# Optimization experiments

Measured on AMD Instinct MI355X. Metric: run time of the kernel, lower is better.

## Reference

```python
import jax, jax.numpy as jnp
import numpy as np
from math import sqrt

N = 50000      # n_nodes
M = 800000     # n_edges (avg degree 16)
D = 256        # d_Embedding
H = 8          # heads
DK = 32        # per-head key/query dim
DV = 32        # per-head value dim


def setup_inputs() -> dict:
    key = jax.random.key(0)
    ks = jax.random.split(key, 10)
    s = 0.02
    x = jax.random.normal(ks[0], (N, D), dtype=jnp.float32)
    edge_index = jax.random.randint(ks[1], (2, M), 0, N, dtype=jnp.int32)
    # projection weights stored pre-reshaped to (D, H, dhead); equivalent to nn.Linear(D, H*dhead)
    Wk = jax.random.normal(ks[2], (D, H, DK), dtype=jnp.float32) * s
    bk = jax.random.normal(ks[3], (H, DK), dtype=jnp.float32) * s
    Wq = jax.random.normal(ks[4], (D, H, DK), dtype=jnp.float32) * s
    bq = jax.random.normal(ks[5], (H, DK), dtype=jnp.float32) * s
    Wv = jax.random.normal(ks[6], (D, H, DV), dtype=jnp.float32) * s
    bv = jax.random.normal(ks[7], (H, DV), dtype=jnp.float32) * s
    Wagg = jax.random.normal(ks[8], (H * DV, D), dtype=jnp.float32) * s
    bagg = jnp.zeros((D,), dtype=jnp.float32)
    Wff = jax.random.normal(ks[9], (D, D), dtype=jnp.float32) * s
    bff = jnp.zeros((D,), dtype=jnp.float32)
    return {"x": x, "edge_index": edge_index, "Wk": Wk, "bk": bk, "Wq": Wq,
            "bq": bq, "Wv": Wv, "bv": bv, "Wagg": Wagg, "bagg": bagg,
            "Wff": Wff, "bff": bff}


def reference(x, edge_index, Wk, bk, Wq, bq, Wv, bv, Wagg, bagg, Wff, bff):
    recv = edge_index[0]
    send = edge_index[1]
    # per-head projections: (N, H, d)
    K = jnp.einsum('nd,dhk->nhk', x, Wk) + bk
    Q = jnp.einsum('nd,dhk->nhk', x, Wq) + bq
    V = jnp.einsum('nd,dhv->nhv', x, Wv) + bv
    # edge-wise attention logits: (M, H)
    qk = jnp.sum(Q[recv] * K[send], axis=-1)
    # faithful to original: rescale by 3/global_max, then exp
    att = jnp.exp(qk * 3.0 / jnp.max(qk))
    # segment-softmax normalization over edges sharing a receiver
    sums = jax.ops.segment_sum(att, recv, num_segments=N)  # (N, H)
    att = att / sums[recv] / sqrt(DK)
    # weighted scatter-add of sender values: (N, H, DV)
    msg = att[..., None] * V[send]
    out = jax.ops.segment_sum(msg, recv, num_segments=N)
    out = jax.nn.relu(out).reshape(N, H * DV)
    out = jax.nn.relu(out @ Wagg + bagg)
    out = jax.nn.relu(out @ Wff + bff)
    return x + out
```

## Files before the change

### kernel.cpp

```cpp
#include <hip/hip_runtime.h>

#define N_NODES 50000
#define M_EDGES 800000

typedef __bf16 bf16x8 __attribute__((ext_vector_type(8)));
typedef __bf16 bf16x4 __attribute__((ext_vector_type(4)));
typedef float  f32x4  __attribute__((ext_vector_type(4)));

static __device__ __forceinline__ unsigned enc_ord(float f) {
    unsigned b = __float_as_uint(f);
    return (b & 0x80000000u) ? ~b : (b | 0x80000000u);
}
static __device__ __forceinline__ float dec_ord(unsigned u) {
    unsigned b = (u & 0x80000000u) ? (u ^ 0x80000000u) : ~u;
    return __uint_as_float(b);
}
static __device__ __forceinline__ float bflo(unsigned u) { return __uint_as_float(u << 16); }
static __device__ __forceinline__ float bfhi(unsigned u) { return __uint_as_float(u & 0xffff0000u); }

__global__ void init_kernel(int* counts, int* cursor, unsigned* gmax) {
    int t = blockIdx.x * blockDim.x + threadIdx.x;
    if (t < N_NODES) { counts[t] = 0; cursor[t] = 0; }
    if (t == 0) *gmax = 0u;
}

__global__ void wsplit_kernel(const float* __restrict__ W,
                              __bf16* __restrict__ th, __bf16* __restrict__ tl) {
    int t = blockIdx.x * 256 + threadIdx.x;
    int n = t >> 8, k = t & 255;
    float v = W[(size_t)k * 256 + n];
    __bf16 h = (__bf16)v;
    th[t] = h;
    tl[t] = (__bf16)(v - (float)h);
}

__global__ __launch_bounds__(256) void gemm_mfma(
    const float* __restrict__ A,
    const __bf16* __restrict__ Bth, const __bf16* __restrict__ Btl,
    const float* __restrict__ bias, const float* __restrict__ residual,
    float* __restrict__ C, __bf16* __restrict__ Cb, int nrows, int do_relu) {
    __shared__ __attribute__((aligned(16))) __bf16 sAh[128 * 40];
    __shared__ __attribute__((aligned(16))) __bf16 sAl[128 * 40];
    __shared__ __attribute__((aligned(16))) __bf16 sBh[128 * 40];
    __shared__ __attribute__((aligned(16))) __bf16 sBl[128 * 40];

    int row0 = blockIdx.x * 128;
    int n0   = blockIdx.y * 128;
    int tid  = threadIdx.x;
    int lane = tid & 63, wave = tid >> 6;
    int wm = (wave >> 1) * 64, wn = (wave & 1) * 64;

    f32x4 acc[4][4];
    #pragma unroll
    for (int i = 0; i < 4; i++)
        #pragma unroll
        for (int j = 0; j < 4; j++) acc[i][j] = (f32x4)(0.f);

    int r  = tid >> 1;
    int hf = tid & 1;

    for (int kk = 0; kk < 256; kk += 32) {
        {
            const float* ap = A + (size_t)(row0 + r) * 256 + kk + hf * 16;
            bool valid = (row0 + r) < nrows;
            #pragma unroll
            for (int q = 0; q < 4; q++) {
                float4 v = valid ? *(const float4*)(ap + q * 4)
                                 : make_float4(0.f, 0.f, 0.f, 0.f);
                bf16x4 hh, ll;
                hh[0] = (__bf16)v.x; ll[0] = (__bf16)(v.x - (float)hh[0]);
                hh[1] = (__bf16)v.y; ll[1] = (__bf16)(v.y - (float)hh[1]);
                hh[2] = (__bf16)v.z; ll[2] = (__bf16)(v.z - (float)hh[2]);
                hh[3] = (__bf16)v.w; ll[3] = (__bf16)(v.w - (float)hh[3]);
                *(bf16x4*)&sAh[r * 40 + hf * 16 + q * 4] = hh;
                *(bf16x4*)&sAl[r * 40 + hf * 16 + q * 4] = ll;
            }
        }
        {
            size_t gb = (size_t)(n0 + r) * 256 + kk + hf * 16;
            uint4 vh0 = *(const uint4*)(Bth + gb);
            uint4 vh1 = *(const uint4*)(Bth + gb + 8);
            uint4 vl0 = *(const uint4*)(Btl + gb);
            uint4 vl1 = *(const uint4*)(Btl + gb + 8);
            *(uint4*)&sBh[r * 40 + hf * 16]     = vh0;
            *(uint4*)&sBh[r * 40 + hf * 16 + 8] = vh1;
            *(uint4*)&sBl[r * 40 + hf * 16]     = vl0;
            *(uint4*)&sBl[r * 40 + hf * 16 + 8] = vl1;
        }
        __syncthreads();

        int m_base = wm + (lane & 15);
        int n_base = wn + (lane & 15);
        int koff = (lane >> 4) * 8;
        bf16x8 ah[4], al[4], bh[4], bl[4];
        #pragma unroll
        for (int mt = 0; mt < 4; mt++) {
            ah[mt] = *(const bf16x8*)&sAh[(m_base + mt * 16) * 40 + koff];
            al[mt] = *(const bf16x8*)&sAl[(m_base + mt * 16) * 40 + koff];
        }
        #pragma unroll
        for (int nt = 0; nt < 4; nt++) {
            bh[nt] = *(const bf16x8*)&sBh[(n_base + nt * 16) * 40 + koff];
            bl[nt] = *(const bf16x8*)&sBl[(n_base + nt * 16) * 40 + koff];
        }
        #pragma unroll
        for (int mt = 0; mt < 4; mt++)
            #pragma unroll
            for (int nt = 0; nt < 4; nt++) {
                acc[mt][nt] = __builtin_amdgcn_mfma_f32_16x16x32_bf16(ah[mt], bh[nt], acc[mt][nt], 0, 0, 0);
                acc[mt][nt] = __builtin_amdgcn_mfma_f32_16x16x32_bf16(al[mt], bh[nt], acc[mt][nt], 0, 0, 0);
                acc[mt][nt] = __builtin_amdgcn_mfma_f32_16x16x32_bf16(ah[mt], bl[nt], acc[mt][nt], 0, 0, 0);
            }
        __syncthreads();
    }

    #pragma unroll
    for (int mt = 0; mt < 4; mt++) {
        #pragma unroll
        for (int nt = 0; nt < 4; nt++) {
            int col = n0 + wn + nt * 16 + (lane & 15);
            #pragma unroll
            for (int rr = 0; rr < 4; rr++) {
                int row = row0 + wm + mt * 16 + (lane >> 4) * 4 + rr;
                if (row < nrows) {
                    float v = acc[mt][nt][rr] + bias[col];
                    if (do_relu) v = fmaxf(v, 0.f);
                    if (Cb) {
                        Cb[(size_t)row * 256 + col] = (__bf16)v;
                    } else {
                        if (residual) v += residual[(size_t)row * 256 + col];
                        C[(size_t)row * 256 + col] = v;
                    }
                }
            }
        }
    }
}

__global__ void hist_kernel(const int* __restrict__ recv, int* __restrict__ counts) {
    int t = blockIdx.x * 256 + threadIdx.x;
    if (t < M_EDGES) atomicAdd(&counts[recv[t]], 1);
}

__global__ void scan_kernel(const int* __restrict__ counts, int* __restrict__ offsets) {
    __shared__ int part[256];
    int t = threadIdx.x;
    const int per = (N_NODES + 255) / 256;
    int start = t * per;
    int end = min(start + per, N_NODES);
    int s = 0;
    for (int i = start; i < end; i++) s += counts[i];
    part[t] = s;
    __syncthreads();
    if (t == 0) {
        int acc = 0;
        for (int i = 0; i < 256; i++) { int v = part[i]; part[i] = acc; acc += v; }
    }
    __syncthreads();
    int acc = part[t];
    for (int i = start; i < end; i++) { offsets[i] = acc; acc += counts[i]; }
    if (end == N_NODES && start < N_NODES) offsets[N_NODES] = acc;
}

__global__ void fill_kernel(const int* __restrict__ recv, const int* __restrict__ send,
                            const int* __restrict__ offsets,
                            int* __restrict__ cursor, int* __restrict__ ssorted,
                            int* __restrict__ rsorted) {
    int t = blockIdx.x * 256 + threadIdx.x;
    if (t < M_EDGES) {
        int r = recv[t];
        int pos = offsets[r] + atomicAdd(&cursor[r], 1);
        ssorted[pos] = send[t];
        rsorted[pos] = r;
    }
}

__global__ __launch_bounds__(256) void qk_csr_kernel(
    const int* __restrict__ ssorted, const int* __restrict__ rsorted,
    const float* __restrict__ Q, const unsigned short* __restrict__ Kb,
    float* __restrict__ qks, unsigned* __restrict__ gmax) {
    int wave_id = (blockIdx.x * 256 + threadIdx.x) >> 6;
    int lane = threadIdx.x & 63;
    int e_slot = lane >> 5;
    int sl = lane & 31;
    const int nwaves = (gridDim.x * 256) >> 6;
    const int npairs = M_EDGES / 2;
    float wmax = -INFINITY;
    for (int pp = wave_id; pp < npairs; pp += 4 * nwaves) {
        int ep[4]; bool valid[4];
        #pragma unroll
        for (int u = 0; u < 4; u++) {
            int p = pp + u * nwaves;
            valid[u] = p < npairs;
            ep[u] = (valid[u] ? p : pp) * 2 + e_slot;
        }
        int si[4], ri[4];
        #pragma unroll
        for (int u = 0; u < 4; u++) { si[u] = ssorted[ep[u]]; ri[u] = rsorted[ep[u]]; }
        uint4 kv[4]; float4 qa[4], qb[4];
        #pragma unroll
        for (int u = 0; u < 4; u++) {
            kv[u] = *(const uint4*)(Kb + (size_t)si[u] * 256 + sl * 8);
            qa[u] = *(const float4*)(Q + (size_t)ri[u] * 256 + sl * 8);
            qb[u] = *(const float4*)(Q + (size_t)ri[u] * 256 + sl * 8 + 4);
        }
        #pragma unroll
        for (int u = 0; u < 4; u++) {
            float d = qa[u].x * bflo(kv[u].x) + qa[u].y * bfhi(kv[u].x)
                    + qa[u].z * bflo(kv[u].y) + qa[u].w * bfhi(kv[u].y)
                    + qb[u].x * bflo(kv[u].z) + qb[u].y * bfhi(kv[u].z)
                    + qb[u].z * bflo(kv[u].w) + qb[u].w * bfhi(kv[u].w);
            d += __shfl_xor(d, 1);
            d += __shfl_xor(d, 2);
            wmax = fmaxf(wmax, d);
            if ((sl & 3) == 0 && valid[u])
                qks[(size_t)ep[u] * 8 + (sl >> 2)] = d;
        }
    }
    wmax = fmaxf(wmax, __shfl_xor(wmax, 1));
    wmax = fmaxf(wmax, __shfl_xor(wmax, 2));
    wmax = fmaxf(wmax, __shfl_xor(wmax, 4));
    wmax = fmaxf(wmax, __shfl_xor(wmax, 8));
    wmax = fmaxf(wmax, __shfl_xor(wmax, 16));
    wmax = fmaxf(wmax, __shfl_xor(wmax, 32));
    if (lane == 0 && wmax > -INFINITY) atomicMax(gmax, enc_ord(wmax));
}

__global__ __launch_bounds__(256) void node_agg_kernel(
    const int* __restrict__ offsets, const int* __restrict__ ssorted,
    const float* __restrict__ qks, const unsigned short* __restrict__ Vb,
    const unsigned* __restrict__ gmax, float* __restrict__ msg) {
    int wave_id = (blockIdx.x * 256 + threadIdx.x) >> 6;
    int lane = threadIdx.x & 63;
    int h = lane >> 3;
    const int nwaves = (gridDim.x * 256) >> 6;
    const int per = (N_NODES + nwaves - 1) / nwaves;
    int n0 = wave_id * per;
    int nend = min(n0 + per, N_NODES);
    float scale = 3.0f / dec_ord(*gmax);
    for (int n = n0; n < nend; n++) {
        int off = offsets[n];
        int deg = offsets[n + 1] - off;
        float sum = 0.f, a0 = 0.f, a1 = 0.f, a2 = 0.f, a3 = 0.f;
        for (int b = 0; b < deg; b += 64) {
            int bn = min(64, deg - b);
            int idxb = ssorted[off + b + min(lane, bn - 1)];
            #define VROW(i) (*(const uint2*)(Vb + \
                (size_t)__shfl(idxb, min((i), bn - 1)) * 256 + lane * 4))
            #define QKL(i) qks[(size_t)(off + b + min((i), bn - 1)) * 8 + h]
            uint2 v0 = VROW(0);
            uint2 v1 = VROW(1);
            float q0 = QKL(0);
            float q1 = QKL(1);
            for (int i = 0; i < bn; i++) {
                uint2 vc = v0; v0 = v1; v1 = VROW(i + 2);
                float qc = q0; q0 = q1; q1 = QKL(i + 2);
                float a = __expf(qc * scale);
                sum += a;
                a0 += a * bflo(vc.x); a1 += a * bfhi(vc.x);
                a2 += a * bflo(vc.y); a3 += a * bfhi(vc.y);
            }
            #undef VROW
            #undef QKL
        }
        float inv = (deg > 0) ? 1.0f / (sum * 5.65685424949238f) : 0.f;
        *(float4*)(msg + (size_t)n * 256 + lane * 4) =
            make_float4(fmaxf(a0 * inv, 0.f), fmaxf(a1 * inv, 0.f),
                        fmaxf(a2 * inv, 0.f), fmaxf(a3 * inv, 0.f));
    }
}

extern "C" void kernel_launch(void* const* d_in, const int* in_sizes, int n_in,
                              void* d_out, int out_size, void* d_ws, size_t ws_size,
                              hipStream_t stream) {
    const float* x    = (const float*)d_in[0];
    const int*   edge = (const int*)d_in[1];
    const int*   recv = edge;
    const int*   send = edge + M_EDGES;
    const float* Wk   = (const float*)d_in[2];
    const float* bk   = (const float*)d_in[3];
    const float* Wq   = (const float*)d_in[4];
    const float* bq   = (const float*)d_in[5];
    const float* Wv   = (const float*)d_in[6];
    const float* bv   = (const float*)d_in[7];
    const float* Wagg = (const float*)d_in[8];
    const float* bagg = (const float*)d_in[9];
    const float* Wff  = (const float*)d_in[10];
    const float* bff  = (const float*)d_in[11];
    float* out = (float*)d_out;

    float*  Qbuf  = (float*)d_ws;
    float*  msg   = Qbuf + (size_t)N_NODES * 256;
    float*  qks   = msg + (size_t)N_NODES * 256;
    __bf16* Kbf   = (__bf16*)(qks + (size_t)M_EDGES * 8);
    __bf16* Vbf   = Kbf + (size_t)N_NODES * 256;
    int* counts   = (int*)(Vbf + (size_t)N_NODES * 256);
    int* cursor   = counts + N_NODES;
    int* offsets  = cursor + N_NODES;
    int* ssorted  = offsets + N_NODES + 1;
    unsigned* gmax = (unsigned*)(ssorted + M_EDGES);
    __bf16* wt    = (__bf16*)(gmax + 1);
    __bf16* WkH = wt;              __bf16* WkL = wt + 65536;
    __bf16* WqH = wt + 2 * 65536;  __bf16* WqL = wt + 3 * 65536;
    __bf16* WvH = wt + 4 * 65536;  __bf16* WvL = wt + 5 * 65536;
    __bf16* WaH = wt + 6 * 65536;  __bf16* WaL = wt + 7 * 65536;
    __bf16* WfH = wt + 8 * 65536;  __bf16* WfL = wt + 9 * 65536;
    int* rsorted  = (int*)msg;
    float* hidden = Qbuf;

    dim3 blk(256);
    dim3 gemm_grid((N_NODES + 127) / 128, 2);
    dim3 edge_grid((M_EDGES + 255) / 256);

    hipLaunchKernelGGL(init_kernel, dim3((N_NODES + 255) / 256), blk, 0, stream,
                       counts, cursor, gmax);
    hipLaunchKernelGGL(wsplit_kernel, dim3(256), blk, 0, stream, Wk,   WkH, WkL);
    hipLaunchKernelGGL(wsplit_kernel, dim3(256), blk, 0, stream, Wq,   WqH, WqL);
    hipLaunchKernelGGL(wsplit_kernel, dim3(256), blk, 0, stream, Wv,   WvH, WvL);
    hipLaunchKernelGGL(wsplit_kernel, dim3(256), blk, 0, stream, Wagg, WaH, WaL);
    hipLaunchKernelGGL(wsplit_kernel, dim3(256), blk, 0, stream, Wff,  WfH, WfL);
    hipLaunchKernelGGL(gemm_mfma, gemm_grid, blk, 0, stream, x, WkH, WkL, bk, nullptr,
                       (float*)nullptr, Kbf, N_NODES, 0);
    hipLaunchKernelGGL(gemm_mfma, gemm_grid, blk, 0, stream, x, WqH, WqL, bq, nullptr,
                       Qbuf, (__bf16*)nullptr, N_NODES, 0);
    hipLaunchKernelGGL(gemm_mfma, gemm_grid, blk, 0, stream, x, WvH, WvL, bv, nullptr,
                       (float*)nullptr, Vbf, N_NODES, 0);
    hipLaunchKernelGGL(hist_kernel, edge_grid, blk, 0, stream, recv, counts);
    hipLaunchKernelGGL(scan_kernel, dim3(1), blk, 0, stream, counts, offsets);
    hipLaunchKernelGGL(fill_kernel, edge_grid, blk, 0, stream, recv, send, offsets,
                       cursor, ssorted, rsorted);
    hipLaunchKernelGGL(qk_csr_kernel, dim3(1024), blk, 0, stream,
                       ssorted, rsorted, Qbuf, (const unsigned short*)Kbf, qks, gmax);
    hipLaunchKernelGGL(node_agg_kernel, dim3(2048), blk, 0, stream,
                       offsets, ssorted, qks, (const unsigned short*)Vbf, gmax, msg);
    hipLaunchKernelGGL(gemm_mfma, gemm_grid, blk, 0, stream, msg, WaH, WaL, bagg, nullptr,
                       hidden, (__bf16*)nullptr, N_NODES, 1);
    hipLaunchKernelGGL(gemm_mfma, gemm_grid, blk, 0, stream, hidden, WfH, WfL, bff, x,
                       out, (__bf16*)nullptr, N_NODES, 1);
}
```

Measured before the change: 845.4 us.

## Compute QK logits per receiver node, reusing Q row across its edges

Replaces the edge-pair QK kernel with a node-centric kernel where each wave walks contiguous CSR segments of receiver nodes, loading the Q row once and reusing it for all incident edges. This removes the rsorted array and its writes in fill_kernel, and cuts repeated fp32 Q gathers per edge. In exchange each wave handles a fixed contiguous node range, so degree imbalance and partial 4-edge batches waste some lanes, and there is less memory-level parallelism per wave.

Measured after the change: 850.3 us. About the same (+0.6%).

```diff
diff --git a/kernel.cpp b/kernel.cpp
--- a/kernel.cpp
+++ b/kernel.cpp
@@ -164,57 +164,53 @@
 
 __global__ void fill_kernel(const int* __restrict__ recv, const int* __restrict__ send,
                             const int* __restrict__ offsets,
-                            int* __restrict__ cursor, int* __restrict__ ssorted,
-                            int* __restrict__ rsorted) {
+                            int* __restrict__ cursor, int* __restrict__ ssorted) {
     int t = blockIdx.x * 256 + threadIdx.x;
     if (t < M_EDGES) {
         int r = recv[t];
         int pos = offsets[r] + atomicAdd(&cursor[r], 1);
         ssorted[pos] = send[t];
-        rsorted[pos] = r;
-    }
-}
-
-__global__ __launch_bounds__(256) void qk_csr_kernel(
-    const int* __restrict__ ssorted, const int* __restrict__ rsorted,
+    }
+}
+
+__global__ __launch_bounds__(256) void qk_node_kernel(
+    const int* __restrict__ offsets, const int* __restrict__ ssorted,
     const float* __restrict__ Q, const unsigned short* __restrict__ Kb,
     float* __restrict__ qks, unsigned* __restrict__ gmax) {
     int wave_id = (blockIdx.x * 256 + threadIdx.x) >> 6;
     int lane = threadIdx.x & 63;
-    int e_slot = lane >> 5;
-    int sl = lane & 31;
     const int nwaves = (gridDim.x * 256) >> 6;
-    const int npairs = M_EDGES / 2;
+    const int per = (N_NODES + nwaves - 1) / nwaves;
+    int n0 = wave_id * per;
+    int nend = min(n0 + per, N_NODES);
+    bool wr = (lane & 7) == 0;
+    int h = lane >> 3;
     float wmax = -INFINITY;
-    for (int pp = wave_id; pp < npairs; pp += 4 * nwaves) {
-        int ep[4]; bool valid[4];
-        #pragma unroll
-        for (int u = 0; u < 4; u++) {
-            int p = pp + u * nwaves;
-            valid[u] = p < npairs;
-            ep[u] = (valid[u] ? p : pp) * 2 + e_slot;
-        }
-        int si[4], ri[4];
-        #pragma unroll
-        for (int u = 0; u < 4; u++) { si[u] = ssorted[ep[u]]; ri[u] = rsorted[ep[u]]; }
-        uint4 kv[4]; float4 qa[4], qb[4];
-        #pragma unroll
-        for (int u = 0; u < 4; u++) {
-            kv[u] = *(const uint4*)(Kb + (size_t)si[u] * 256 + sl * 8);
-            qa[u] = *(const float4*)(Q + (size_t)ri[u] * 256 + sl * 8);
-            qb[u] = *(const float4*)(Q + (size_t)ri[u] * 256 + sl * 8 + 4);
-        }
-        #pragma unroll
-        for (int u = 0; u < 4; u++) {
-            float d = qa[u].x * bflo(kv[u].x) + qa[u].y * bfhi(kv[u].x)
-                    + qa[u].z * bflo(kv[u].y) + qa[u].w * bfhi(kv[u].y)
-                    + qb[u].x * bflo(kv[u].z) + qb[u].y * bfhi(kv[u].z)
-                    + qb[u].z * bflo(kv[u].w) + qb[u].w * bfhi(kv[u].w);
-            d += __shfl_xor(d, 1);
-            d += __shfl_xor(d, 2);
-            wmax = fmaxf(wmax, d);
-            if ((sl & 3) == 0 && valid[u])
-                qks[(size_t)ep[u] * 8 + (sl >> 2)] = d;
+    for (int n = n0; n < nend; n++) {
+        int off = offsets[n];
+        int deg = offsets[n + 1] - off;
+        if (deg == 0) continue;
+        float4 q = *(const float4*)(Q + (size_t)n * 256 + lane * 4);
+        for (int b = 0; b < deg; b += 4) {
+            int bn = deg - b;
+            int s[4];
+            #pragma unroll
+            for (int u = 0; u < 4; u++)
+                s[u] = ssorted[off + b + min(u, bn - 1)];
+            uint2 kv[4];
+            #pragma unroll
+            for (int u = 0; u < 4; u++)
+                kv[u] = *(const uint2*)(Kb + (size_t)s[u] * 256 + lane * 4);
+            #pragma unroll
+            for (int u = 0; u < 4; u++) {
+                float d = q.x * bflo(kv[u].x) + q.y * bfhi(kv[u].x)
+                        + q.z * bflo(kv[u].y) + q.w * bfhi(kv[u].y);
+                d += __shfl_xor(d, 1);
+                d += __shfl_xor(d, 2);
+                d += __shfl_xor(d, 4);
+                wmax = fmaxf(wmax, d);
+                if (wr && u < bn) qks[(size_t)(off + b + u) * 8 + h] = d;
+            }
         }
     }
     wmax = fmaxf(wmax, __shfl_xor(wmax, 1));
@@ -305,7 +301,6 @@
     __bf16* WvH = wt + 4 * 65536;  __bf16* WvL = wt + 5 * 65536;
     __bf16* WaH = wt + 6 * 65536;  __bf16* WaL = wt + 7 * 65536;
     __bf16* WfH = wt + 8 * 65536;  __bf16* WfL = wt + 9 * 65536;
-    int* rsorted  = (int*)msg;
     float* hidden = Qbuf;
 
     dim3 blk(256);
@@ -328,9 +323,9 @@
     hipLaunchKernelGGL(hist_kernel, edge_grid, blk, 0, stream, recv, counts);
     hipLaunchKernelGGL(scan_kernel, dim3(1), blk, 0, stream, counts, offsets);
     hipLaunchKernelGGL(fill_kernel, edge_grid, blk, 0, stream, recv, send, offsets,
-                       cursor, ssorted, rsorted);
-    hipLaunchKernelGGL(qk_csr_kernel, dim3(1024), blk, 0, stream,
-                       ssorted, rsorted, Qbuf, (const unsigned short*)Kbf, qks, gmax);
+                       cursor, ssorted);
+    hipLaunchKernelGGL(qk_node_kernel, dim3(2048), blk, 0, stream,
+                       offsets, ssorted, Qbuf, (const unsigned short*)Kbf, qks, gmax);
     hipLaunchKernelGGL(node_agg_kernel, dim3(2048), blk, 0, stream,
                        offsets, ssorted, qks, (const unsigned short*)Vbf, gmax, msg);
     hipLaunchKernelGGL(gemm_mfma, gemm_grid, blk, 0, stream, msg, WaH, WaL, bagg, nullptr,
```

## Pre-split GEMM A operands into bf16 hi/lo planes produced by upstream kernels

Applied to the files above, without the earlier changes.

The GEMM no longer reads fp32 A and splits it into bf16 hi/lo inside every tile load. A new xsplit kernel splits x once for the three projections, and node_agg and the Wagg GEMM now write their outputs directly as hi/lo bf16 planes. This avoids repeating the split for each of the two column blocks and three projection GEMMs, and lets the A tile be loaded with plain vector copies. In exchange it adds one extra pass over x and rearranges workspace buffers, which now depend on careful aliasing (rsorted, msg and xh share the same region).

Result: no change. 851.4 us (+0.7%).

```diff
diff --git a/kernel.cpp b/kernel.cpp
--- a/kernel.cpp
+++ b/kernel.cpp
@@ -2,6 +2,7 @@
 
 #define N_NODES 50000
 #define M_EDGES 800000
+#define RP 50048
 
 typedef __bf16 bf16x8 __attribute__((ext_vector_type(8)));
 typedef __bf16 bf16x4 __attribute__((ext_vector_type(4)));
@@ -34,11 +35,26 @@
     tl[t] = (__bf16)(v - (float)h);
 }
 
+__global__ void xsplit_kernel(const float* __restrict__ X,
+                              __bf16* __restrict__ xh, __bf16* __restrict__ xl) {
+    size_t i = ((size_t)blockIdx.x * 256 + threadIdx.x) * 4;
+    if (i >= (size_t)N_NODES * 256) return;
+    float4 v = *(const float4*)(X + i);
+    bf16x4 hh, ll;
+    hh[0] = (__bf16)v.x; ll[0] = (__bf16)(v.x - (float)hh[0]);
+    hh[1] = (__bf16)v.y; ll[1] = (__bf16)(v.y - (float)hh[1]);
+    hh[2] = (__bf16)v.z; ll[2] = (__bf16)(v.z - (float)hh[2]);
+    hh[3] = (__bf16)v.w; ll[3] = (__bf16)(v.w - (float)hh[3]);
+    *(bf16x4*)(xh + i) = hh;
+    *(bf16x4*)(xl + i) = ll;
+}
+
 __global__ __launch_bounds__(256) void gemm_mfma(
-    const float* __restrict__ A,
+    const __bf16* __restrict__ Ah, const __bf16* __restrict__ Al,
     const __bf16* __restrict__ Bth, const __bf16* __restrict__ Btl,
     const float* __restrict__ bias, const float* __restrict__ residual,
-    float* __restrict__ C, __bf16* __restrict__ Cb, int nrows, int do_relu) {
+    float* __restrict__ C, __bf16* __restrict__ CbH, __bf16* __restrict__ CbL,
+    int nrows, int do_relu) {
     __shared__ __attribute__((aligned(16))) __bf16 sAh[128 * 40];
     __shared__ __attribute__((aligned(16))) __bf16 sAl[128 * 40];
     __shared__ __attribute__((aligned(16))) __bf16 sBh[128 * 40];
@@ -58,23 +74,20 @@
 
     int r  = tid >> 1;
     int hf = tid & 1;
+    bool valid = (row0 + r) < nrows;
 
     for (int kk = 0; kk < 256; kk += 32) {
         {
-            const float* ap = A + (size_t)(row0 + r) * 256 + kk + hf * 16;
-            bool valid = (row0 + r) < nrows;
-            #pragma unroll
-            for (int q = 0; q < 4; q++) {
-                float4 v = valid ? *(const float4*)(ap + q * 4)
-                                 : make_float4(0.f, 0.f, 0.f, 0.f);
-                bf16x4 hh, ll;
-                hh[0] = (__bf16)v.x; ll[0] = (__bf16)(v.x - (float)hh[0]);
-                hh[1] = (__bf16)v.y; ll[1] = (__bf16)(v.y - (float)hh[1]);
-                hh[2] = (__bf16)v.z; ll[2] = (__bf16)(v.z - (float)hh[2]);
-                hh[3] = (__bf16)v.w; ll[3] = (__bf16)(v.w - (float)hh[3]);
-                *(bf16x4*)&sAh[r * 40 + hf * 16 + q * 4] = hh;
-                *(bf16x4*)&sAl[r * 40 + hf * 16 + q * 4] = ll;
-            }
+            size_t ga = (size_t)(row0 + r) * 256 + kk + hf * 16;
+            uint4 z = make_uint4(0u, 0u, 0u, 0u);
+            uint4 ah0 = valid ? *(const uint4*)(Ah + ga)     : z;
+            uint4 ah1 = valid ? *(const uint4*)(Ah + ga + 8) : z;
+            uint4 al0 = valid ? *(const uint4*)(Al + ga)     : z;
+            uint4 al1 = valid ? *(const uint4*)(Al + ga + 8) : z;
+            *(uint4*)&sAh[r * 40 + hf * 16]     = ah0;
+            *(uint4*)&sAh[r * 40 + hf * 16 + 8] = ah1;
+            *(uint4*)&sAl[r * 40 + hf * 16]     = al0;
+            *(uint4*)&sAl[r * 40 + hf * 16 + 8] = al1;
         }
         {
             size_t gb = (size_t)(n0 + r) * 256 + kk + hf * 16;
@@ -125,11 +138,14 @@
                 if (row < nrows) {
                     float v = acc[mt][nt][rr] + bias[col];
                     if (do_relu) v = fmaxf(v, 0.f);
-                    if (Cb) {
-                        Cb[(size_t)row * 256 + col] = (__bf16)v;
+                    size_t idx = (size_t)row * 256 + col;
+                    if (CbH) {
+                        __bf16 hh = (__bf16)v;
+                        CbH[idx] = hh;
+                        if (CbL) CbL[idx] = (__bf16)(v - (float)hh);
                     } else {
-                        if (residual) v += residual[(size_t)row * 256 + col];
-                        C[(size_t)row * 256 + col] = v;
+                        if (residual) v += residual[idx];
+                        C[idx] = v;
                     }
                 }
             }
@@ -229,7 +245,8 @@
 __global__ __launch_bounds__(256) void node_agg_kernel(
     const int* __restrict__ offsets, const int* __restrict__ ssorted,
     const float* __restrict__ qks, const unsigned short* __restrict__ Vb,
-    const unsigned* __restrict__ gmax, float* __restrict__ msg) {
+    const unsigned* __restrict__ gmax,
+    __bf16* __restrict__ msgH, __bf16* __restrict__ msgL) {
     int wave_id = (blockIdx.x * 256 + threadIdx.x) >> 6;
     int lane = threadIdx.x & 63;
     int h = lane >> 3;
@@ -264,9 +281,15 @@
             #undef QKL
         }
         float inv = (deg > 0) ? 1.0f / (sum * 5.65685424949238f) : 0.f;
-        *(float4*)(msg + (size_t)n * 256 + lane * 4) =
-            make_float4(fmaxf(a0 * inv, 0.f), fmaxf(a1 * inv, 0.f),
-                        fmaxf(a2 * inv, 0.f), fmaxf(a3 * inv, 0.f));
+        float r0 = fmaxf(a0 * inv, 0.f), r1 = fmaxf(a1 * inv, 0.f);
+        float r2 = fmaxf(a2 * inv, 0.f), r3 = fmaxf(a3 * inv, 0.f);
+        bf16x4 hv, lv;
+        hv[0] = (__bf16)r0; lv[0] = (__bf16)(r0 - (float)hv[0]);
+        hv[1] = (__bf16)r1; lv[1] = (__bf16)(r1 - (float)hv[1]);
+        hv[2] = (__bf16)r2; lv[2] = (__bf16)(r2 - (float)hv[2]);
+        hv[3] = (__bf16)r3; lv[3] = (__bf16)(r3 - (float)hv[3]);
+        *(bf16x4*)(msgH + (size_t)n * 256 + lane * 4) = hv;
+        *(bf16x4*)(msgL + (size_t)n * 256 + lane * 4) = lv;
     }
 }
 
@@ -290,11 +313,11 @@
     float* out = (float*)d_out;
 
     float*  Qbuf  = (float*)d_ws;
-    float*  msg   = Qbuf + (size_t)N_NODES * 256;
-    float*  qks   = msg + (size_t)N_NODES * 256;
+    float*  reg2  = Qbuf + (size_t)RP * 256;
+    float*  qks   = reg2 + (size_t)RP * 256;
     __bf16* Kbf   = (__bf16*)(qks + (size_t)M_EDGES * 8);
-    __bf16* Vbf   = Kbf + (size_t)N_NODES * 256;
-    int* counts   = (int*)(Vbf + (size_t)N_NODES * 256);
+    __bf16* Vbf   = Kbf + (size_t)RP * 256;
+    int* counts   = (int*)(Vbf + (size_t)RP * 256);
     int* cursor   = counts + N_NODES;
     int* offsets  = cursor + N_NODES;
     int* ssorted  = offsets + N_NODES + 1;
@@ -305,8 +328,13 @@
     __bf16* WvH = wt + 4 * 65536;  __bf16* WvL = wt + 5 * 65536;
     __bf16* WaH = wt + 6 * 65536;  __bf16* WaL = wt + 7 * 65536;
     __bf16* WfH = wt + 8 * 65536;  __bf16* WfL = wt + 9 * 65536;
-    int* rsorted  = (int*)msg;
-    float* hidden = Qbuf;
+    __bf16* xh   = (__bf16*)reg2;
+    __bf16* xl   = xh + (size_t)RP * 256;
+    int*    rsorted = (int*)reg2;
+    __bf16* msgH = (__bf16*)reg2;
+    __bf16* msgL = msgH + (size_t)RP * 256;
+    __bf16* hidH = (__bf16*)Qbuf;
+    __bf16* hidL = hidH + (size_t)RP * 256;
 
     dim3 blk(256);
     dim3 gemm_grid((N_NODES + 127) / 128, 2);
@@ -319,12 +347,14 @@
     hipLaunchKernelGGL(wsplit_kernel, dim3(256), blk, 0, stream, Wv,   WvH, WvL);
     hipLaunchKernelGGL(wsplit_kernel, dim3(256), blk, 0, stream, Wagg, WaH, WaL);
     hipLaunchKernelGGL(wsplit_kernel, dim3(256), blk, 0, stream, Wff,  WfH, WfL);
-    hipLaunchKernelGGL(gemm_mfma, gemm_grid, blk, 0, stream, x, WkH, WkL, bk, nullptr,
-                       (float*)nullptr, Kbf, N_NODES, 0);
-    hipLaunchKernelGGL(gemm_mfma, gemm_grid, blk, 0, stream, x, WqH, WqL, bq, nullptr,
-                       Qbuf, (__bf16*)nullptr, N_NODES, 0);
-    hipLaunchKernelGGL(gemm_mfma, gemm_grid, blk, 0, stream, x, WvH, WvL, bv, nullptr,
-                       (float*)nullptr, Vbf, N_NODES, 0);
+    hipLaunchKernelGGL(xsplit_kernel, dim3((N_NODES * 256 / 4 + 255) / 256), blk, 0,
+                       stream, x, xh, xl);
+    hipLaunchKernelGGL(gemm_mfma, gemm_grid, blk, 0, stream, xh, xl, WkH, WkL, bk,
+                       nullptr, (float*)nullptr, Kbf, (__bf16*)nullptr, N_NODES, 0);
+    hipLaunchKernelGGL(gemm_mfma, gemm_grid, blk, 0, stream, xh, xl, WqH, WqL, bq,
+                       nullptr, Qbuf, (__bf16*)nullptr, (__bf16*)nullptr, N_NODES, 0);
+    hipLaunchKernelGGL(gemm_mfma, gemm_grid, blk, 0, stream, xh, xl, WvH, WvL, bv,
+                       nullptr, (float*)nullptr, Vbf, (__bf16*)nullptr, N_NODES, 0);
     hipLaunchKernelGGL(hist_kernel, edge_grid, blk, 0, stream, recv, counts);
     hipLaunchKernelGGL(scan_kernel, dim3(1), blk, 0, stream, counts, offsets);
     hipLaunchKernelGGL(fill_kernel, edge_grid, blk, 0, stream, recv, send, offsets,
@@ -332,9 +362,10 @@
     hipLaunchKernelGGL(qk_csr_kernel, dim3(1024), blk, 0, stream,
                        ssorted, rsorted, Qbuf, (const unsigned short*)Kbf, qks, gmax);
     hipLaunchKernelGGL(node_agg_kernel, dim3(2048), blk, 0, stream,
-                       offsets, ssorted, qks, (const unsigned short*)Vbf, gmax, msg);
-    hipLaunchKernelGGL(gemm_mfma, gemm_grid, blk, 0, stream, msg, WaH, WaL, bagg, nullptr,
-                       hidden, (__bf16*)nullptr, N_NODES, 1);
-    hipLaunchKernelGGL(gemm_mfma, gemm_grid, blk, 0, stream, hidden, WfH, WfL, bff, x,
-                       out, (__bf16*)nullptr, N_NODES, 1);
-}
+                       offsets, ssorted, qks, (const unsigned short*)Vbf, gmax,
+                       msgH, msgL);
+    hipLaunchKernelGGL(gemm_mfma, gemm_grid, blk, 0, stream, msgH, msgL, WaH, WaL,
+                       bagg, nullptr, (float*)nullptr, hidH, hidL, N_NODES, 1);
+    hipLaunchKernelGGL(gemm_mfma, gemm_grid, blk, 0, stream, hidH, hidL, WfH, WfL,
+                       bff, x, out, (__bf16*)nullptr, (__bf16*)nullptr, N_NODES, 1);
+}
```
